# Optimization experiments

Measured on AMD Instinct MI355X. Metric: run time of the kernel, lower is better.

Reference implementation:

```python
import jax, jax.numpy as jnp
import numpy as np

B, L, D = 128, 196, 1024  # batch, att_size, rnn_size


def setup_inputs() -> dict:
    key = jax.random.key(0)
    ks = jax.random.split(key, 11)
    s = 1.0 / np.sqrt(D)
    return {
        "x": jax.random.normal(ks[0], (B, D), jnp.float32),
        "att": jax.random.normal(ks[1], (B, L, D), jnp.float32),
        "h": jax.random.normal(ks[2], (B, D), jnp.float32),
        "W_a2a": jax.random.uniform(ks[3], (D, D), jnp.float32, -s, s),
        "b_a2a": jax.random.uniform(ks[4], (D,), jnp.float32, -s, s),
        "W_h2a": jax.random.uniform(ks[5], (D, D), jnp.float32, -s, s),
        "b_h2a": jax.random.uniform(ks[6], (D,), jnp.float32, -s, s),
        "W_i2a": jax.random.uniform(ks[7], (D, D), jnp.float32, -s, s),
        "b_i2a": jax.random.uniform(ks[8], (D,), jnp.float32, -s, s),
        "W_d2d": jax.random.uniform(ks[9], (D,), jnp.float32, -s, s),
        "b_d2d": jax.random.uniform(ks[10], (), jnp.float32, -s, s),
    }


def reference(x, att, h, W_a2a, b_a2a, W_h2a, b_h2a, W_i2a, b_i2a, W_d2d, b_d2d):
    # att_v_1: [B, L, D]
    att_v = jnp.einsum('bld,ed->ble', att, W_a2a) + b_a2a
    att_h = (h @ W_h2a.T + b_h2a)[:, None, :]   # [B, 1, D]
    att_x = (x @ W_i2a.T + b_i2a)[:, None, :]   # [B, 1, D]
    dot = jnp.tanh(att_v + att_h + att_x)       # [B, L, D]
    scores = jnp.einsum('bld,d->bl', dot, W_d2d) + b_d2d  # [B, L]
    weight = jax.nn.softmax(scores, axis=-1)    # [B, L]
    att_res = jnp.einsum('bld,bl->bd', att, weight)  # [B, D]
    return att_res
```

## Files before the change

kernel.cpp:

```cpp
#include <hip/hip_runtime.h>
#include <hip/hip_bf16.h>

#define B_ 128
#define L_ 196
#define D_ 1024
#define M_ (B_*L_)

typedef __attribute__((ext_vector_type(8))) short short8v;
typedef __attribute__((ext_vector_type(4))) float f32x4;
typedef unsigned short ushort_t;

#define OFF_ATTBF   0UL
#define OFF_WBF     51380224UL
#define OFF_A2      53477376UL
#define OFF_W2      54001664UL
#define OFF_C       58195968UL
#define OFF_SPART   58720256UL

__device__ inline unsigned short f2bf(float f) {
  unsigned int u = __float_as_uint(f);
  unsigned int r = (u + 0x7fffu + ((u >> 16) & 1u)) >> 16;
  return (unsigned short)r;
}

__global__ void convert_kernel(const float* __restrict__ att, const float* __restrict__ Wa,
                               const float* __restrict__ x,   const float* __restrict__ h,
                               const float* __restrict__ Wi,  const float* __restrict__ Wh,
                               ushort_t* __restrict__ att_bf, ushort_t* __restrict__ W_bf,
                               ushort_t* __restrict__ A2,     ushort_t* __restrict__ W2) {
  const int n0 = (B_*L_*D_)/4;
  const int n1 = (D_*D_)/4;
  const int n2 = (B_*D_)/4;
  const int total = n0 + n1 + 2*n2 + 2*n1;
  for (int idx = blockIdx.x*blockDim.x + threadIdx.x; idx < total;
       idx += gridDim.x*blockDim.x) {
    const float4* src; ushort_t* dst;
    int i = idx;
    if (i < n0)               { src = (const float4*)att + i; dst = att_bf + (size_t)i*4; }
    else if ((i -= n0) < n1)  { src = (const float4*)Wa  + i; dst = W_bf  + (size_t)i*4; }
    else if ((i -= n1) < n2)  { int b = i>>8, k4 = i&255; src = (const float4*)x  + i; dst = A2 + b*2048 + k4*4; }
    else if ((i -= n2) < n2)  { int b = i>>8, k4 = i&255; src = (const float4*)h  + i; dst = A2 + b*2048 + 1024 + k4*4; }
    else if ((i -= n2) < n1)  { int e = i>>8, k4 = i&255; src = (const float4*)Wi + i; dst = W2 + e*2048 + k4*4; }
    else { i -= n1;             int e = i>>8, k4 = i&255; src = (const float4*)Wh + i; dst = W2 + e*2048 + 1024 + k4*4; }
    float4 v = *src;
    ushort4 o; o.x = f2bf(v.x); o.y = f2bf(v.y); o.z = f2bf(v.z); o.w = f2bf(v.w);
    *(ushort4*)dst = o;
  }
}

__device__ inline void stage_tile(const ushort_t* __restrict__ g, int row0, int K, int k0,
                                  ushort_t* ldst, int t) {
  #pragma unroll
  for (int it = 0; it < 4; ++it) {
    int linear = it*4096 + t*16;
    int r = linear >> 7;
    int c = (t & 7) ^ (r & 7);
    const ushort_t* src = g + (size_t)(row0 + r)*K + k0 + c*8;
    ushort_t* dst = ldst + ((it*4096 + ((t & 192) << 4)) >> 1);
    __builtin_amdgcn_global_load_lds((const __attribute__((address_space(1))) void*)src,
                                     (__attribute__((address_space(3))) void*)dst,
                                     16, 0, 0);
  }
}

__device__ inline short8v ldfrag(const ushort_t* tile, int row, int c) {
  int phys = c ^ (row & 7);
  return *(const short8v*)(tile + row*64 + phys*8);
}

template<int EPI>
__global__ __launch_bounds__(256) void gemm_kernel(
    const ushort_t* __restrict__ Amat, const ushort_t* __restrict__ Bmat, int K,
    const float* __restrict__ ba, const float* __restrict__ bh, const float* __restrict__ bi,
    const float* __restrict__ cmat, const float* __restrict__ wd,
    float* __restrict__ outc, float* __restrict__ spart) {
  __shared__ ushort_t lds[32768];
  int bid = blockIdx.x;
  int nwg = gridDim.x;
  int cpx = nwg >> 3;
  int swz = (bid & 7)*cpx + (bid >> 3);
  int m_blk = swz >> 3, e_blk = swz & 7;
  int m0 = m_blk*128, e0 = e_blk*128;
  int t = threadIdx.x, lane = t & 63, w = t >> 6;
  int wm = w >> 1, we = w & 1;
  int lrow = lane & 15;
  int lk = lane >> 4;

  f32x4 acc[4][4];
  #pragma unroll
  for (int i = 0; i < 4; ++i)
    #pragma unroll
    for (int j = 0; j < 4; ++j) acc[i][j] = (f32x4){0.f, 0.f, 0.f, 0.f};

  stage_tile(Amat, m0, K, 0, lds, t);
  stage_tile(Bmat, e0, K, 0, lds + 8192, t);
  __syncthreads();

  int nk = K >> 6;
  for (int kt = 0; kt < nk; ++kt) {
    int cur = kt & 1;
    if (kt + 1 < nk) {
      stage_tile(Amat, m0, K, (kt+1) << 6, lds + (cur^1)*16384, t);
      stage_tile(Bmat, e0, K, (kt+1) << 6, lds + (cur^1)*16384 + 8192, t);
    }
    const ushort_t* At = lds + cur*16384;
    const ushort_t* Bt = At + 8192;
    #pragma unroll
    for (int hh = 0; hh < 2; ++hh) {
      short8v af[4], bfv[4];
      #pragma unroll
      for (int i = 0; i < 4; ++i) af[i]  = ldfrag(At, wm*64 + i*16 + lrow, hh*4 + lk);
      #pragma unroll
      for (int j = 0; j < 4; ++j) bfv[j] = ldfrag(Bt, we*64 + j*16 + lrow, hh*4 + lk);
      #pragma unroll
      for (int i = 0; i < 4; ++i)
        #pragma unroll
        for (int j = 0; j < 4; ++j)
          acc[i][j] = __builtin_amdgcn_mfma_f32_16x16x32_bf16(af[i], bfv[j], acc[i][j], 0, 0, 0);
    }
    __syncthreads();
  }

  if (EPI == 0) {
    #pragma unroll
    for (int i = 0; i < 4; ++i) {
      int m = m0 + wm*64 + i*16 + lk*4;
      #pragma unroll
      for (int j = 0; j < 4; ++j) {
        int e = e0 + we*64 + j*16 + lrow;
        float bsum = ba[e] + bh[e] + bi[e];
        #pragma unroll
        for (int r = 0; r < 4; ++r)
          outc[(m + r)*1024 + e] = acc[i][j][r] + bsum;
      }
    }
  } else {
    #pragma unroll
    for (int i = 0; i < 4; ++i) {
      #pragma unroll
      for (int r = 0; r < 4; ++r) {
        int m = m0 + wm*64 + i*16 + lk*4 + r;
        int bb = (int)((unsigned)m / 196u);
        float partial = 0.f;
        #pragma unroll
        for (int j = 0; j < 4; ++j) {
          int e = e0 + we*64 + j*16 + lrow;
          float v = acc[i][j][r] + cmat[bb*1024 + e];
          float ex = __expf(2.f*v);
          partial += (1.f - 2.f/(ex + 1.f)) * wd[e];
        }
        #pragma unroll
        for (int off = 1; off < 16; off <<= 1)
          partial += __shfl_xor(partial, off);
        if (lrow == 0)
          spart[(size_t)m*16 + e_blk*2 + we] = partial;
      }
    }
  }
}

__global__ __launch_bounds__(256) void finalize_kernel(const float* __restrict__ att,
                                                       const float* __restrict__ spart,
                                                       float* __restrict__ out) {
  int b  = blockIdx.x >> 1;
  int dh = blockIdx.x & 1;
  int t  = threadIdx.x;
  __shared__ float wls[L_];
  __shared__ float red[8];

  float s = -1e30f;
  if (t < L_) {
    const float* sp = spart + (size_t)(b*L_ + t)*16;
    float sum = 0.f;
    #pragma unroll
    for (int p = 0; p < 16; ++p) sum += sp[p];
    s = sum;
  }
  float m = s;
  #pragma unroll
  for (int off = 1; off < 64; off <<= 1) m = fmaxf(m, __shfl_xor(m, off));
  if ((t & 63) == 0) red[t >> 6] = m;
  __syncthreads();
  m = fmaxf(fmaxf(red[0], red[1]), fmaxf(red[2], red[3]));
  float p = (t < L_) ? __expf(s - m) : 0.f;
  float ssum = p;
  #pragma unroll
  for (int off = 1; off < 64; off <<= 1) ssum += __shfl_xor(ssum, off);
  if ((t & 63) == 0) red[4 + (t >> 6)] = ssum;
  __syncthreads();
  float tot = red[4] + red[5] + red[6] + red[7];
  if (t < L_) wls[t] = p / tot;
  __syncthreads();

  int d = dh*512 + t*2;
  const float* abase = att + (size_t)b*L_*D_ + d;
  float a0 = 0.f, a1 = 0.f;
  #pragma unroll 4
  for (int l = 0; l < L_; ++l) {
    float wv = wls[l];
    float2 av = *(const float2*)(abase + (size_t)l*D_);
    a0 += wv*av.x; a1 += wv*av.y;
  }
  float2 o; o.x = a0; o.y = a1;
  *(float2*)(out + (size_t)b*D_ + d) = o;
}

extern "C" void kernel_launch(void* const* d_in, const int* in_sizes, int n_in,
                              void* d_out, int out_size, void* d_ws, size_t ws_size,
                              hipStream_t stream) {
  (void)in_sizes; (void)n_in; (void)out_size; (void)ws_size;
  const float* x   = (const float*)d_in[0];
  const float* att = (const float*)d_in[1];
  const float* h   = (const float*)d_in[2];
  const float* Wa  = (const float*)d_in[3];
  const float* ba  = (const float*)d_in[4];
  const float* Wh  = (const float*)d_in[5];
  const float* bh  = (const float*)d_in[6];
  const float* Wi  = (const float*)d_in[7];
  const float* bi  = (const float*)d_in[8];
  const float* wd  = (const float*)d_in[9];

  char* ws = (char*)d_ws;
  ushort_t* att_bf = (ushort_t*)(ws + OFF_ATTBF);
  ushort_t* W_bf   = (ushort_t*)(ws + OFF_WBF);
  ushort_t* A2     = (ushort_t*)(ws + OFF_A2);
  ushort_t* W2     = (ushort_t*)(ws + OFF_W2);
  float*    cmat   = (float*)(ws + OFF_C);
  float*    spart  = (float*)(ws + OFF_SPART);
  float*    out    = (float*)d_out;

  hipLaunchKernelGGL(convert_kernel, dim3(2048), dim3(256), 0, stream,
                     att, Wa, x, h, Wi, Wh, att_bf, W_bf, A2, W2);
  hipLaunchKernelGGL(gemm_kernel<0>, dim3(8), dim3(256), 0, stream,
                     A2, W2, 2048, ba, bh, bi, (const float*)nullptr, wd, cmat, (float*)nullptr);
  hipLaunchKernelGGL(gemm_kernel<1>, dim3(1568), dim3(256), 0, stream,
                     att_bf, W_bf, 1024, ba, bh, bi, cmat, wd, (float*)nullptr, spart);
  hipLaunchKernelGGL(finalize_kernel, dim3(256), dim3(256), 0, stream,
                     att, spart, out);
}
```

Baseline: 153.0 us.

## Rewrite score GEMM as 256x256-tile 8-wave kernel with interleaved prefetch schedule

Splits the templated GEMM into a small kernel for the h/x projection and a dedicated score kernel. The score kernel uses 256x256 output tiles, 512 threads and double-buffered LDS staged in half-tiles. Global-to-LDS prefetch is interleaved between MFMA phases, using explicit barriers, waitcnt and setprio to overlap loads with compute and raise reuse per loaded byte. This costs more registers and 128KB of LDS per block, and the grid drops to 392 blocks, so wave-quantisation and occupancy could suffer.

```diff
diff --git a/kernel.cpp b/kernel.cpp
--- a/kernel.cpp
+++ b/kernel.cpp
@@ -4,7 +4,6 @@
 #define B_ 128
 #define L_ 196
 #define D_ 1024
-#define M_ (B_*L_)
 
 typedef __attribute__((ext_vector_type(8))) short short8v;
 typedef __attribute__((ext_vector_type(4))) float f32x4;
@@ -68,19 +67,13 @@
   return *(const short8v*)(tile + row*64 + phys*8);
 }
 
-template<int EPI>
-__global__ __launch_bounds__(256) void gemm_kernel(
+__global__ __launch_bounds__(256) void gemm_c_kernel(
     const ushort_t* __restrict__ Amat, const ushort_t* __restrict__ Bmat, int K,
     const float* __restrict__ ba, const float* __restrict__ bh, const float* __restrict__ bi,
-    const float* __restrict__ cmat, const float* __restrict__ wd,
-    float* __restrict__ outc, float* __restrict__ spart) {
+    float* __restrict__ outc) {
   __shared__ ushort_t lds[32768];
   int bid = blockIdx.x;
-  int nwg = gridDim.x;
-  int cpx = nwg >> 3;
-  int swz = (bid & 7)*cpx + (bid >> 3);
-  int m_blk = swz >> 3, e_blk = swz & 7;
-  int m0 = m_blk*128, e0 = e_blk*128;
+  int m0 = 0, e0 = (bid & 7)*128;
   int t = threadIdx.x, lane = t & 63, w = t >> 6;
   int wm = w >> 1, we = w & 1;
   int lrow = lane & 15;
@@ -121,40 +114,147 @@
     __syncthreads();
   }
 
-  if (EPI == 0) {
-    #pragma unroll
-    for (int i = 0; i < 4; ++i) {
-      int m = m0 + wm*64 + i*16 + lk*4;
+  #pragma unroll
+  for (int i = 0; i < 4; ++i) {
+    int m = m0 + wm*64 + i*16 + lk*4;
+    #pragma unroll
+    for (int j = 0; j < 4; ++j) {
+      int e = e0 + we*64 + j*16 + lrow;
+      float bsum = ba[e] + bh[e] + bi[e];
+      #pragma unroll
+      for (int r = 0; r < 4; ++r)
+        outc[(m + r)*1024 + e] = acc[i][j][r] + bsum;
+    }
+  }
+}
+
+__device__ inline short8v ldfrag2(const ushort_t* tile, int row, int c) {
+  int phys = c ^ (row & 7);
+  return *(const short8v*)(tile + row*64 + phys*8);
+}
+
+__device__ inline void stage_half(const ushort_t* __restrict__ g, int row0, int Kdim,
+                                  int kt, int half, ushort_t* lds_tile, int t, int w) {
+  #pragma unroll
+  for (int it2 = 0; it2 < 2; ++it2) {
+    int linear = it2*8192 + t*16;
+    int r = linear >> 7;
+    int pc = (linear >> 4) & 7;
+    int c = pc ^ (r & 7);
+    const ushort_t* src = g + (size_t)(row0 + half*128 + r)*Kdim + kt*64 + c*8;
+    ushort_t* dst = lds_tile + half*8192 + it2*4096 + w*512;
+    __builtin_amdgcn_global_load_lds((const __attribute__((address_space(1))) void*)src,
+                                     (__attribute__((address_space(3))) void*)dst,
+                                     16, 0, 0);
+  }
+}
+
+#define SB0()   __builtin_amdgcn_sched_barrier(0)
+#define BARR()  __builtin_amdgcn_s_barrier()
+#define LGKM0() asm volatile("s_waitcnt lgkmcnt(0)" ::: "memory")
+#define VM6()   asm volatile("s_waitcnt vmcnt(6)" ::: "memory")
+
+#define RD_A_LO(base) { _Pragma("unroll") for (int i_=0;i_<4;++i_) { int rr = wm*64 + i_*16 + lrow; \
+    a[i_][0]=ldfrag2(base, rr, lk); a[i_][1]=ldfrag2(base, rr, 4+lk);} }
+#define RD_A_HI(base) { _Pragma("unroll") for (int i_=0;i_<4;++i_) { int rr = 128 + wm*64 + i_*16 + lrow; \
+    a[i_][0]=ldfrag2(base, rr, lk); a[i_][1]=ldfrag2(base, rr, 4+lk);} }
+#define RD_B_LO(base) { _Pragma("unroll") for (int j_=0;j_<2;++j_) { int rr = wn*64 + j_*16 + lrow; \
+    b[j_][0]=ldfrag2(base, rr, lk); b[j_][1]=ldfrag2(base, rr, 4+lk);} }
+#define RD_B_HI(base) { _Pragma("unroll") for (int j_=0;j_<2;++j_) { int rr = wn*64 + (2+j_)*16 + lrow; \
+    b[2+j_][0]=ldfrag2(base, rr, lk); b[2+j_][1]=ldfrag2(base, rr, 4+lk);} }
+
+#define MFMAQ(I0, J0) { _Pragma("unroll") for (int i_=0;i_<4;++i_) { _Pragma("unroll") for (int j_=0;j_<2;++j_) { \
+    acc[(I0)+i_][(J0)+j_] = __builtin_amdgcn_mfma_f32_16x16x32_bf16(a[i_][0], b[(J0)+j_][0], acc[(I0)+i_][(J0)+j_], 0,0,0); \
+    acc[(I0)+i_][(J0)+j_] = __builtin_amdgcn_mfma_f32_16x16x32_bf16(a[i_][1], b[(J0)+j_][1], acc[(I0)+i_][(J0)+j_], 0,0,0); } } }
+
+#define PH_TAIL(I0, J0) SB0(); BARR(); LGKM0(); SB0(); \
+    __builtin_amdgcn_s_setprio(1); MFMAQ(I0, J0); __builtin_amdgcn_s_setprio(0); SB0(); BARR();
+
+__global__ __launch_bounds__(512, 2) void gemm_score_kernel(
+    const ushort_t* __restrict__ Amat, const ushort_t* __restrict__ Bmat,
+    const float* __restrict__ cmat, const float* __restrict__ wd,
+    float* __restrict__ spart) {
+  __shared__ ushort_t lds[65536];
+  const int K = 1024, nk = 16, NI = 8;
+  int bid = blockIdx.x;
+  int swz = (bid & 7)*49 + (bid >> 3);
+  int m_blk = swz >> 2, e_blk = swz & 3;
+  int m0 = m_blk*256, e0 = e_blk*256;
+  int t = (int)threadIdx.x, lane = t & 63, w = t >> 6;
+  int wm = w >> 2, wn = w & 3;
+  int lrow = lane & 15, lk = lane >> 4;
+
+  ushort_t* A0_ = lds;
+  ushort_t* B0_ = lds + 16384;
+  ushort_t* A1_ = lds + 32768;
+  ushort_t* B1_ = lds + 49152;
+
+  f32x4 acc[8][4];
+  #pragma unroll
+  for (int i = 0; i < 8; ++i)
+    #pragma unroll
+    for (int j = 0; j < 4; ++j) acc[i][j] = (f32x4){0.f, 0.f, 0.f, 0.f};
+  short8v a[4][2], b[4][2];
+
+  stage_half(Amat, m0, K, 0, 0, A0_, t, w);
+  stage_half(Amat, m0, K, 0, 1, A0_, t, w);
+  stage_half(Bmat, e0, K, 0, 0, B0_, t, w);
+  stage_half(Bmat, e0, K, 0, 1, B0_, t, w);
+  stage_half(Amat, m0, K, 1, 0, A1_, t, w);
+  stage_half(Bmat, e0, K, 1, 0, B1_, t, w);
+  stage_half(Bmat, e0, K, 1, 1, B1_, t, w);
+  VM6(); SB0(); BARR();
+
+  for (int itr = 0; itr < NI; ++itr) {
+    int kt0 = 2*itr;
+    int kc2 = (kt0+2 < nk) ? kt0+2 : nk-1;
+    int kc3 = (kt0+3 < nk) ? kt0+3 : nk-1;
+    RD_A_LO(A0_); RD_B_LO(B0_);
+    stage_half(Amat, m0, K, kt0+1, 1, A1_, t, w);
+    PH_TAIL(0,0);
+    RD_B_HI(B0_);
+    stage_half(Amat, m0, K, kc2, 0, A0_, t, w);
+    PH_TAIL(0,2);
+    RD_A_HI(A0_);
+    stage_half(Bmat, e0, K, kc2, 0, B0_, t, w);
+    PH_TAIL(4,0);
+    stage_half(Bmat, e0, K, kc2, 1, B0_, t, w);
+    VM6();
+    PH_TAIL(4,2);
+    RD_A_LO(A1_); RD_B_LO(B1_);
+    stage_half(Amat, m0, K, kc2, 1, A0_, t, w);
+    PH_TAIL(0,0);
+    RD_B_HI(B1_);
+    stage_half(Amat, m0, K, kc3, 0, A1_, t, w);
+    PH_TAIL(0,2);
+    RD_A_HI(A1_);
+    stage_half(Bmat, e0, K, kc3, 0, B1_, t, w);
+    PH_TAIL(4,0);
+    stage_half(Bmat, e0, K, kc3, 1, B1_, t, w);
+    VM6();
+    PH_TAIL(4,2);
+  }
+
+  #pragma unroll
+  for (int i = 0; i < 8; ++i) {
+    int mbase = m0 + (i>>2)*128 + wm*64 + (i&3)*16 + lk*4;
+    #pragma unroll
+    for (int r = 0; r < 4; ++r) {
+      int m = mbase + r;
+      int bb = (int)((unsigned)m / 196u);
+      float partial = 0.f;
       #pragma unroll
       for (int j = 0; j < 4; ++j) {
-        int e = e0 + we*64 + j*16 + lrow;
-        float bsum = ba[e] + bh[e] + bi[e];
-        #pragma unroll
-        for (int r = 0; r < 4; ++r)
-          outc[(m + r)*1024 + e] = acc[i][j][r] + bsum;
+        int e = e0 + wn*64 + j*16 + lrow;
+        float v = acc[i][j][r] + cmat[bb*1024 + e];
+        float ex = __expf(2.f*v);
+        partial += (1.f - 2.f/(ex + 1.f)) * wd[e];
       }
-    }
-  } else {
-    #pragma unroll
-    for (int i = 0; i < 4; ++i) {
-      #pragma unroll
-      for (int r = 0; r < 4; ++r) {
-        int m = m0 + wm*64 + i*16 + lk*4 + r;
-        int bb = (int)((unsigned)m / 196u);
-        float partial = 0.f;
-        #pragma unroll
-        for (int j = 0; j < 4; ++j) {
-          int e = e0 + we*64 + j*16 + lrow;
-          float v = acc[i][j][r] + cmat[bb*1024 + e];
-          float ex = __expf(2.f*v);
-          partial += (1.f - 2.f/(ex + 1.f)) * wd[e];
-        }
-        #pragma unroll
-        for (int off = 1; off < 16; off <<= 1)
-          partial += __shfl_xor(partial, off);
-        if (lrow == 0)
-          spart[(size_t)m*16 + e_blk*2 + we] = partial;
-      }
+      partial += __shfl_xor(partial, 1);
+      partial += __shfl_xor(partial, 2);
+      partial += __shfl_xor(partial, 4);
+      partial += __shfl_xor(partial, 8);
+      if (lrow == 0) spart[(size_t)m*16 + e_blk*4 + wn] = partial;
     }
   }
 }
@@ -231,10 +331,10 @@
 
   hipLaunchKernelGGL(convert_kernel, dim3(2048), dim3(256), 0, stream,
                      att, Wa, x, h, Wi, Wh, att_bf, W_bf, A2, W2);
-  hipLaunchKernelGGL(gemm_kernel<0>, dim3(8), dim3(256), 0, stream,
-                     A2, W2, 2048, ba, bh, bi, (const float*)nullptr, wd, cmat, (float*)nullptr);
-  hipLaunchKernelGGL(gemm_kernel<1>, dim3(1568), dim3(256), 0, stream,
-                     att_bf, W_bf, 1024, ba, bh, bi, cmat, wd, (float*)nullptr, spart);
+  hipLaunchKernelGGL(gemm_c_kernel, dim3(8), dim3(256), 0, stream,
+                     A2, W2, 2048, ba, bh, bi, cmat);
+  hipLaunchKernelGGL(gemm_score_kernel, dim3(392), dim3(512), 0, stream,
+                     att_bf, W_bf, cmat, wd, spart);
   hipLaunchKernelGGL(finalize_kernel, dim3(256), dim3(256), 0, stream,
                      att, spart, out);
 }
```

Result: slower. 157.0 us (+2.6%).
